# Kernel tuning notes

Hardware: AMD Instinct MI355X
Metric: run time of the kernel (lower is better)

Reference implementation:

```python
import jax, jax.numpy as jnp
import numpy as np

EPS = 1e-5


def _layernorm(x, w, b):
    mu = jnp.mean(x, axis=-1, keepdims=True)
    var = jnp.var(x, axis=-1, keepdims=True)
    return (x - mu) * jax.lax.rsqrt(var + EPS) * w + b


def setup_inputs() -> dict:
    key = jax.random.key(0)
    ks = jax.random.split(key, 3)
    h, dff = 1024, 4096
    x = jax.random.normal(ks[0], (4, 2048, h), dtype=jnp.float32)
    w1 = jax.random.normal(ks[1], (h, dff), dtype=jnp.float32) * (1.0 / np.sqrt(h))
    w2 = jax.random.normal(ks[2], (dff, h), dtype=jnp.float32) * (1.0 / np.sqrt(dff))
    return {
        "x": x,
        "ln1_w": jnp.ones((h,), jnp.float32),
        "ln1_b": jnp.zeros((h,), jnp.float32),
        "ln2_w": jnp.ones((h,), jnp.float32),
        "ln2_b": jnp.zeros((h,), jnp.float32),
        "w1": w1,
        "b1": jnp.zeros((dff,), jnp.float32),
        "w2": w2,
        "b2": jnp.zeros((h,), jnp.float32),
    }


def reference(x, ln1_w, ln1_b, ln2_w, ln2_b, w1, b1, w2, b2):
    # double 1D FFT: over hidden (dim=-1) then sequence (dim=-2), keep real part
    fourier_x = jnp.fft.fft(jnp.fft.fft(x, axis=-1), axis=-2).real
    x = x + fourier_x
    x = _layernorm(x, ln1_w, ln1_b)
    # FFN: Linear -> exact GELU -> Linear (dropout is identity in eval)
    h = jax.nn.gelu(jnp.einsum("bsd,df->bsf", x, w1) + b1, approximate=False)
    x = x + jnp.einsum("bsf,fd->bsd", h, w2) + b2
    return _layernorm(x, ln2_w, ln2_b)
```

## Files before the change

kernel.cpp:

```cpp
#include <hip/hip_runtime.h>
#include <hip/hip_bf16.h>
#include <math.h>

typedef __bf16 bf16_t;
typedef __bf16 bf16x8 __attribute__((ext_vector_type(8)));
typedef __bf16 bf16x4 __attribute__((ext_vector_type(4)));
typedef float  f32x4  __attribute__((ext_vector_type(4)));

#define NROWS 8192
#define HD    1024
#define DFF   4096
#define HKEEP 544

typedef __attribute__((address_space(1))) const void* gas_cptr;
typedef __attribute__((address_space(3))) void* las_ptr;

__device__ __forceinline__ void gload_lds16(const void* g, void* l) {
  __builtin_amdgcn_global_load_lds((gas_cptr)g, (las_ptr)l, 16, 0, 0);
}

__global__ __launch_bounds__(256) void transpose_to_bf16(
    const float* __restrict__ in, bf16_t* __restrict__ out, int R, int C)
{
  __shared__ float tile[32][33];
  const int bx = blockIdx.x, by = blockIdx.y;
  const int tx = threadIdx.x, ty = threadIdx.y;
  #pragma unroll
  for (int i = ty; i < 32; i += 8)
    tile[i][tx] = in[(size_t)(by*32 + i)*C + bx*32 + tx];
  __syncthreads();
  #pragma unroll
  for (int i = ty; i < 32; i += 8)
    out[(size_t)(bx*32 + i)*R + by*32 + tx] = (bf16_t)tile[tx][i];
}

__global__ __launch_bounds__(256) void fft_h_kernel(
    const float* __restrict__ x, float* __restrict__ re, float* __restrict__ im)
{
  __shared__ float sre[1024], sim[1024], twc[512], tws[512];
  const int t = threadIdx.x;
  const size_t row = blockIdx.x;
  const float* xr = x + row * HD;
  for (int k = t; k < 512; k += 256) {
    float sv, cv; sincosf(-6.28318530717958647692f * (float)k * (1.0f/1024.0f), &sv, &cv);
    twc[k] = cv; tws[k] = sv;
  }
  #pragma unroll
  for (int q = 0; q < 4; ++q) sre[t + 256*q] = xr[t + 256*q];
  __syncthreads();
  float rv[4];
  #pragma unroll
  for (int q = 0; q < 4; ++q) rv[q] = sre[__brev((unsigned)(t + 256*q)) >> 22];
  __syncthreads();
  #pragma unroll
  for (int q = 0; q < 4; ++q) { sre[t + 256*q] = rv[q]; sim[t + 256*q] = 0.0f; }
  __syncthreads();
  for (int s = 0; s < 10; ++s) {
    const int half = 1 << s;
    #pragma unroll
    for (int q = 0; q < 2; ++q) {
      const int b  = t + 256*q;
      const int j  = b & (half - 1);
      const int ib = ((b >> s) << (s + 1)) | j;
      const int ti2 = j << (9 - s);
      const float wc = twc[ti2], ws = tws[ti2];
      const float r1 = sre[ib],       i1v = sim[ib];
      const float r2 = sre[ib+half],  i2v = sim[ib+half];
      const float tr = r2*wc - i2v*ws;
      const float ti = r2*ws + i2v*wc;
      sre[ib]      = r1 + tr; sim[ib]      = i1v + ti;
      sre[ib+half] = r1 - tr; sim[ib+half] = i1v - ti;
    }
    __syncthreads();
  }
  #pragma unroll
  for (int q = 0; q < 4; ++q) {
    const int idx = t + 256*q;
    if (idx < HKEEP) {
      re[row*HD + idx] = sre[idx];
      im[row*HD + idx] = sim[idx];
    }
  }
}

__global__ __launch_bounds__(256) void transpose2_f32(
    const float* __restrict__ re, const float* __restrict__ im,
    float* __restrict__ reT, float* __restrict__ imT)
{
  __shared__ float t0[32][33], t1[32][33];
  const int h0 = blockIdx.x * 32;
  const int b0 = blockIdx.y * 32;
  const int tx = threadIdx.x, ty = threadIdx.y;
  #pragma unroll
  for (int i = ty; i < 32; i += 8) {
    t0[i][tx] = re[(size_t)(b0+i)*HD + h0+tx];
    t1[i][tx] = im[(size_t)(b0+i)*HD + h0+tx];
  }
  __syncthreads();
  #pragma unroll
  for (int i = ty; i < 32; i += 8) {
    reT[(size_t)(h0+i)*NROWS + b0+tx] = t0[tx][i];
    imT[(size_t)(h0+i)*NROWS + b0+tx] = t1[tx][i];
  }
}

__global__ __launch_bounds__(256) void fft_s_col(
    const float* __restrict__ reT, const float* __restrict__ imT,
    float* __restrict__ fT)
{
  __shared__ float sre[2048], sim[2048], twc[1024], tws[1024];
  const int t = threadIdx.x;
  const int h = blockIdx.x;
  const int batch = blockIdx.y;
  const size_t base = (size_t)h * NROWS + batch * 2048;
  for (int k = t; k < 1024; k += 256) {
    float sv, cv; sincosf(-6.28318530717958647692f * (float)k * (1.0f/2048.0f), &sv, &cv);
    twc[k] = cv; tws[k] = sv;
  }
  #pragma unroll
  for (int q = 0; q < 8; ++q) {
    const int i = t + 256*q;
    const int src = __brev((unsigned)i) >> 21;
    sre[i] = reT[base + src];
    sim[i] = imT[base + src];
  }
  __syncthreads();
  for (int s = 0; s < 11; ++s) {
    const int half = 1 << s;
    #pragma unroll
    for (int q = 0; q < 4; ++q) {
      const int b  = t + 256*q;
      const int j  = b & (half - 1);
      const int ib = ((b >> s) << (s + 1)) | j;
      const int ti2 = j << (10 - s);
      const float wc = twc[ti2], ws = tws[ti2];
      const float r1 = sre[ib],       i1v = sim[ib];
      const float r2 = sre[ib+half],  i2v = sim[ib+half];
      const float tr = r2*wc - i2v*ws;
      const float ti = r2*ws + i2v*wc;
      sre[ib]      = r1 + tr; sim[ib]      = i1v + ti;
      sre[ib+half] = r1 - tr; sim[ib+half] = i1v - ti;
    }
    __syncthreads();
  }
  #pragma unroll
  for (int q = 0; q < 8; ++q) {
    const int i = t + 256*q;
    fT[base + i] = sre[i];
  }
}

__global__ __launch_bounds__(256) void umadd_kernel(
    const float* __restrict__ fT, const float* __restrict__ x,
    float* __restrict__ y)
{
  __shared__ float tile[32][33];
  const int h0 = blockIdx.x * 32;
  const int b0 = blockIdx.y * 32;
  const int tx = threadIdx.x, ty = threadIdx.y;
  const int batch = b0 >> 11;
  const int s0    = b0 & 2047;
  #pragma unroll
  for (int i = ty; i < 32; i += 8) {
    const int h = h0 + i;
    float v;
    if (h <= 512) {
      v = fT[(size_t)h * NROWS + b0 + tx];
    } else {
      const int sp = (2048 - (s0 + tx)) & 2047;
      v = fT[(size_t)(1024 - h) * NROWS + (batch << 11) + sp];
    }
    tile[i][tx] = v;
  }
  __syncthreads();
  #pragma unroll
  for (int i = ty; i < 32; i += 8) {
    const size_t gi = (size_t)(b0+i)*HD + h0+tx;
    y[gi] = x[gi] + tile[tx][i];
  }
}

template <bool OUT_BF16>
__global__ __launch_bounds__(256) void layernorm_k(
    const float* __restrict__ in, const float* __restrict__ gw,
    const float* __restrict__ gb, bf16_t* __restrict__ ob, float* __restrict__ of)
{
  __shared__ float red[8];
  const size_t row = blockIdx.x;
  const int t = threadIdx.x;
  const float* xr = in + row * HD;
  float4 v = *(const float4*)(xr + t*4);
  float s = v.x + v.y + v.z + v.w;
  #pragma unroll
  for (int o = 32; o > 0; o >>= 1) s += __shfl_xor(s, o);
  if ((t & 63) == 0) red[t >> 6] = s;
  __syncthreads();
  const float mu = (red[0]+red[1]+red[2]+red[3]) * (1.0f/1024.0f);
  const float dx = v.x-mu, dy = v.y-mu, dz = v.z-mu, dw = v.w-mu;
  float sq = dx*dx + dy*dy + dz*dz + dw*dw;
  #pragma unroll
  for (int o = 32; o > 0; o >>= 1) sq += __shfl_xor(sq, o);
  if ((t & 63) == 0) red[4 + (t >> 6)] = sq;
  __syncthreads();
  const float var  = (red[4]+red[5]+red[6]+red[7]) * (1.0f/1024.0f);
  const float rstd = rsqrtf(var + 1e-5f);
  const float4 wv = *(const float4*)(gw + t*4);
  const float4 bv = *(const float4*)(gb + t*4);
  const float o0 = dx*rstd*wv.x + bv.x;
  const float o1 = dy*rstd*wv.y + bv.y;
  const float o2 = dz*rstd*wv.z + bv.z;
  const float o3 = dw*rstd*wv.w + bv.w;
  if constexpr (OUT_BF16) {
    bf16x4 o; o[0]=(bf16_t)o0; o[1]=(bf16_t)o1; o[2]=(bf16_t)o2; o[3]=(bf16_t)o3;
    *(bf16x4*)(ob + row*HD + t*4) = o;
  } else {
    float4 o; o.x=o0; o.y=o1; o.z=o2; o.w=o3;
    *(float4*)(of + row*HD + t*4) = o;
  }
}

__device__ __forceinline__ float gelu_exact(float v) {
  return 0.5f * v * (1.0f + erff(v * 0.70710678118654752440f));
}

template <bool GELU_BF16_OUT>
__global__ __launch_bounds__(256) void gemm_bf16_kernel(
    const bf16_t* __restrict__ A,
    const bf16_t* __restrict__ Bt,
    const float*  __restrict__ bias,
    const bf16_t* __restrict__ resid,
    bf16_t* __restrict__ outB, float* __restrict__ outF,
    int M, int N, int K, int gx)
{
  constexpr int BK = 64;
  __shared__ bf16_t As[128*BK];
  __shared__ bf16_t Bs[128*BK];
  const int tid  = threadIdx.x;
  const int wave = tid >> 6, lane = tid & 63;
  const int wr = wave >> 1, wc = wave & 1;
  const int lr  = lane & 15;
  const int lkg = lane >> 4;

  const int nwg = gridDim.x;
  const int sid = (blockIdx.x & 7) * (nwg >> 3) + (blockIdx.x >> 3);
  const int bx = sid % gx, by = sid / gx;
  const int brow = by * 128, bcol = bx * 128;

  const int rloc = lane >> 3;
  const int sgrp = (lane & 7) ^ rloc;
  const bf16_t* Ag = A  + (size_t)(brow + wave*32 + rloc) * K + sgrp * 8;
  const bf16_t* Bg = Bt + (size_t)(bcol + wave*32 + rloc) * K + sgrp * 8;

  f32x4 acc[4][4] = {};

  for (int k0 = 0; k0 < K; k0 += BK) {
    #pragma unroll
    for (int q = 0; q < 4; ++q) {
      gload_lds16(Ag + (size_t)(q*8)*K + k0, &As[(wave*4 + q) * 512]);
      gload_lds16(Bg + (size_t)(q*8)*K + k0, &Bs[(wave*4 + q) * 512]);
    }
    __syncthreads();

    #pragma unroll
    for (int ks = 0; ks < 2; ++ks) {
      const int g = (lkg + ks*4) ^ (lr & 7);
      bf16x8 af[4], bv[4];
      #pragma unroll
      for (int m = 0; m < 4; ++m)
        af[m] = *(const bf16x8*)&As[(wr*64 + m*16 + lr)*BK + g*8];
      #pragma unroll
      for (int n = 0; n < 4; ++n)
        bv[n] = *(const bf16x8*)&Bs[(wc*64 + n*16 + lr)*BK + g*8];
      #pragma unroll
      for (int m = 0; m < 4; ++m)
        #pragma unroll
        for (int n = 0; n < 4; ++n)
          acc[m][n] = __builtin_amdgcn_mfma_f32_16x16x32_bf16(bv[n], af[m], acc[m][n], 0, 0, 0);
    }
    __syncthreads();
  }

  #pragma unroll
  for (int m = 0; m < 4; ++m) {
    const int row = brow + wr*64 + m*16 + lr;
    #pragma unroll
    for (int n = 0; n < 4; ++n) {
      const int col = bcol + wc*64 + n*16 + lkg*4;
      const float4 bv4 = *(const float4*)(bias + col);
      float v0 = acc[m][n][0] + bv4.x;
      float v1 = acc[m][n][1] + bv4.y;
      float v2 = acc[m][n][2] + bv4.z;
      float v3 = acc[m][n][3] + bv4.w;
      if constexpr (GELU_BF16_OUT) {
        bf16x4 o;
        o[0] = (bf16_t)gelu_exact(v0); o[1] = (bf16_t)gelu_exact(v1);
        o[2] = (bf16_t)gelu_exact(v2); o[3] = (bf16_t)gelu_exact(v3);
        *(bf16x4*)(outB + (size_t)row * N + col) = o;
      } else {
        bf16x4 rr = *(const bf16x4*)(resid + (size_t)row * N + col);
        float4 o;
        o.x = v0 + (float)rr[0]; o.y = v1 + (float)rr[1];
        o.z = v2 + (float)rr[2]; o.w = v3 + (float)rr[3];
        *(float4*)(outF + (size_t)row * N + col) = o;
      }
    }
  }
}

extern "C" void kernel_launch(void* const* d_in, const int* in_sizes, int n_in,
                              void* d_out, int out_size, void* d_ws, size_t ws_size,
                              hipStream_t stream) {
  const float* x    = (const float*)d_in[0];
  const float* ln1w = (const float*)d_in[1];
  const float* ln1b = (const float*)d_in[2];
  const float* ln2w = (const float*)d_in[3];
  const float* ln2b = (const float*)d_in[4];
  const float* w1   = (const float*)d_in[5];
  const float* b1   = (const float*)d_in[6];
  const float* w2   = (const float*)d_in[7];
  const float* b2   = (const float*)d_in[8];
  float* out = (float*)d_out;

  char* ws = (char*)d_ws;
  bf16_t* w1b = (bf16_t*)(ws);
  bf16_t* w2b = (bf16_t*)(ws + (8u  << 20));
  float*  re  = (float*) (ws + (16u << 20));
  float*  im  = (float*) (ws + (48u << 20));
  float*  reT = (float*) (ws + (80u << 20));
  float*  imT = (float*) (ws + (98u << 20));
  float*  fT  = (float*) (ws + (16u << 20));
  float*  y   = (float*) (ws + (33u << 20));
  bf16_t* xn  = (bf16_t*)(ws + (16u << 20));
  bf16_t* hg  = (bf16_t*)(ws + (64u << 20));

  transpose_to_bf16<<<dim3(DFF/32, HD/32), dim3(32, 8), 0, stream>>>(w1, w1b, HD, DFF);
  transpose_to_bf16<<<dim3(HD/32, DFF/32), dim3(32, 8), 0, stream>>>(w2, w2b, DFF, HD);

  fft_h_kernel<<<NROWS, 256, 0, stream>>>(x, re, im);

  transpose2_f32<<<dim3(HKEEP/32, NROWS/32), dim3(32, 8), 0, stream>>>(re, im, reT, imT);

  fft_s_col<<<dim3(513, 4), 256, 0, stream>>>(reT, imT, fT);

  umadd_kernel<<<dim3(HD/32, NROWS/32), dim3(32, 8), 0, stream>>>(fT, x, y);

  layernorm_k<true><<<NROWS, 256, 0, stream>>>(y, ln1w, ln1b, xn, nullptr);

  gemm_bf16_kernel<true><<<(DFF/128)*(NROWS/128), 256, 0, stream>>>(
      xn, w1b, b1, nullptr, hg, nullptr, NROWS, DFF, HD, DFF/128);
  gemm_bf16_kernel<false><<<(HD/128)*(NROWS/128), 256, 0, stream>>>(
      hg, w2b, b2, xn, nullptr, out, NROWS, HD, DFF, HD/128);

  layernorm_k<false><<<NROWS, 256, 0, stream>>>(out, ln2w, ln2b, nullptr, out);
}
```

Before: 332.1 us.

## Rewrite FFN GEMMs as 8-wave double-buffered pipelined kernel with larger tiles

```diff
diff --git a/kernel.cpp b/kernel.cpp
--- a/kernel.cpp
+++ b/kernel.cpp
@@ -223,8 +223,8 @@
   return 0.5f * v * (1.0f + erff(v * 0.70710678118654752440f));
 }
 
-template <bool GELU_BF16_OUT>
-__global__ __launch_bounds__(256) void gemm_bf16_kernel(
+template <int NFRAG, bool GELU_OUT>
+__global__ __launch_bounds__(512, 2) void gemm8_kernel(
     const bf16_t* __restrict__ A,
     const bf16_t* __restrict__ Bt,
     const float*  __restrict__ bias,
@@ -232,66 +232,106 @@
     bf16_t* __restrict__ outB, float* __restrict__ outF,
     int M, int N, int K, int gx)
 {
-  constexpr int BK = 64;
-  __shared__ bf16_t As[128*BK];
-  __shared__ bf16_t Bs[128*BK];
+  constexpr int BN = NFRAG * 64;
+  constexpr int BH = BN / 2;
+  __shared__ bf16_t As[2][256 * 64];
+  __shared__ bf16_t Bs[2][BN * 64];
+
   const int tid  = threadIdx.x;
   const int wave = tid >> 6, lane = tid & 63;
-  const int wr = wave >> 1, wc = wave & 1;
-  const int lr  = lane & 15;
-  const int lkg = lane >> 4;
+  const int wr = wave >> 2, wc = wave & 3;
+  const int lr = lane & 15, lkg = lane >> 4;
 
   const int nwg = gridDim.x;
   const int sid = (blockIdx.x & 7) * (nwg >> 3) + (blockIdx.x >> 3);
   const int bx = sid % gx, by = sid / gx;
-  const int brow = by * 128, bcol = bx * 128;
-
-  const int rloc = lane >> 3;
-  const int sgrp = (lane & 7) ^ rloc;
-  const bf16_t* Ag = A  + (size_t)(brow + wave*32 + rloc) * K + sgrp * 8;
-  const bf16_t* Bg = Bt + (size_t)(bcol + wave*32 + rloc) * K + sgrp * 8;
-
-  f32x4 acc[4][4] = {};
-
-  for (int k0 = 0; k0 < K; k0 += BK) {
+  const int brow = by * 256, bcol = bx * BN;
+
+  const int rl = lane >> 3;
+  const int sg = (lane & 7) ^ rl;
+  const bf16_t* Abase = A  + (size_t)(brow + wave*8 + rl) * K + sg*8;
+  const bf16_t* Bbase = Bt + (size_t)(bcol + wave*8 + rl) * K + sg*8;
+
+  auto stageA = [&](int b, int h, int t) {
+    const bf16_t* g = Abase + (size_t)(h*128) * K + t*64;
+    bf16_t* l = &As[b][(h*128 + wave*8) * 64];
+    gload_lds16(g, l);
+    gload_lds16(g + (size_t)64 * K, l + 64*64);
+  };
+  auto stageB = [&](int b, int h, int t) {
+    const bf16_t* g = Bbase + (size_t)(h*BH) * K + t*64;
+    bf16_t* l = &Bs[b][(h*BH + wave*8) * 64];
+    gload_lds16(g, l);
+    if constexpr (NFRAG == 4)
+      gload_lds16(g + (size_t)64 * K, l + 64*64);
+  };
+
+  f32x4 acc[8][NFRAG] = {};
+  bf16x8 af[4], bv[NFRAG];
+
+  const int NT = K >> 6;
+  const int NI = NT >> 1;
+
+  stageA(0,0,0); stageA(0,1,0); stageB(0,0,0); stageB(0,1,0);
+  stageA(1,0,1); stageA(1,1,1); stageB(1,0,1); stageB(1,1,1);
+  asm volatile("s_waitcnt vmcnt(0)" ::: "memory");
+  __builtin_amdgcn_s_barrier();
+
+  #define RD_B(BUF, KS) _Pragma("unroll") \
+      for (int n = 0; n < NFRAG; ++n) { \
+        const int r = wc*(NFRAG*16) + n*16 + lr; \
+        bv[n] = *(const bf16x8*)&Bs[BUF][r*64 + (((lkg + KS*4) ^ (lr & 7))*8)]; }
+  #define RD_A(BUF, MH, KS) _Pragma("unroll") \
+      for (int m = 0; m < 4; ++m) { \
+        const int r = wr*128 + (MH*4 + m)*16 + lr; \
+        af[m] = *(const bf16x8*)&As[BUF][r*64 + (((lkg + KS*4) ^ (lr & 7))*8)]; }
+  #define MFMA_Q(MH) __builtin_amdgcn_s_setprio(1); \
+      _Pragma("unroll") \
+      for (int m = 0; m < 4; ++m) { \
+        _Pragma("unroll") \
+        for (int n = 0; n < NFRAG; ++n) \
+          acc[MH*4 + m][n] = __builtin_amdgcn_mfma_f32_16x16x32_bf16(bv[n], af[m], acc[MH*4 + m][n], 0, 0, 0); } \
+      __builtin_amdgcn_s_setprio(0);
+  #define BAR() __builtin_amdgcn_s_barrier()
+  #define LGKM0() asm volatile("s_waitcnt lgkmcnt(0)" ::: "memory")
+  #define VMW() do { if constexpr (NFRAG == 4) asm volatile("s_waitcnt vmcnt(2)" ::: "memory"); \
+                     else                      asm volatile("s_waitcnt vmcnt(1)" ::: "memory"); } while(0)
+
+  for (int j = 0; j < NI; ++j) {
+    const int t1 = 2*j + 1;
+    const int t2 = (2*j + 2 < NT) ? 2*j + 2 : NT - 1;
+    const int t3 = (2*j + 3 < NT) ? 2*j + 3 : NT - 1;
+
+    RD_B(0,0); RD_A(0,0,0); stageB(1,1,t1);
+    BAR(); LGKM0(); MFMA_Q(0); BAR();
+    RD_A(0,1,0); stageA(1,0,t1);
+    BAR(); LGKM0(); MFMA_Q(1); BAR();
+    RD_B(0,1); RD_A(0,0,1); stageA(1,1,t1);
+    BAR(); LGKM0(); MFMA_Q(0); BAR();
+    RD_A(0,1,1); stageB(0,0,t2);
+    BAR(); LGKM0(); MFMA_Q(1); VMW(); BAR();
+    RD_B(1,0); RD_A(1,0,0); stageB(0,1,t2);
+    BAR(); LGKM0(); MFMA_Q(0); BAR();
+    RD_A(1,1,0); stageA(0,0,t2);
+    BAR(); LGKM0(); MFMA_Q(1); BAR();
+    RD_B(1,1); RD_A(1,0,1); stageA(0,1,t2);
+    BAR(); LGKM0(); MFMA_Q(0); BAR();
+    RD_A(1,1,1); stageB(1,0,t3);
+    BAR(); LGKM0(); MFMA_Q(1); VMW(); BAR();
+  }
+
+  #pragma unroll
+  for (int m = 0; m < 8; ++m) {
+    const int row = brow + wr*128 + m*16 + lr;
     #pragma unroll
-    for (int q = 0; q < 4; ++q) {
-      gload_lds16(Ag + (size_t)(q*8)*K + k0, &As[(wave*4 + q) * 512]);
-      gload_lds16(Bg + (size_t)(q*8)*K + k0, &Bs[(wave*4 + q) * 512]);
-    }
-    __syncthreads();
-
-    #pragma unroll
-    for (int ks = 0; ks < 2; ++ks) {
-      const int g = (lkg + ks*4) ^ (lr & 7);
-      bf16x8 af[4], bv[4];
-      #pragma unroll
-      for (int m = 0; m < 4; ++m)
-        af[m] = *(const bf16x8*)&As[(wr*64 + m*16 + lr)*BK + g*8];
-      #pragma unroll
-      for (int n = 0; n < 4; ++n)
-        bv[n] = *(const bf16x8*)&Bs[(wc*64 + n*16 + lr)*BK + g*8];
-      #pragma unroll
-      for (int m = 0; m < 4; ++m)
-        #pragma unroll
-        for (int n = 0; n < 4; ++n)
-          acc[m][n] = __builtin_amdgcn_mfma_f32_16x16x32_bf16(bv[n], af[m], acc[m][n], 0, 0, 0);
-    }
-    __syncthreads();
-  }
-
-  #pragma unroll
-  for (int m = 0; m < 4; ++m) {
-    const int row = brow + wr*64 + m*16 + lr;
-    #pragma unroll
-    for (int n = 0; n < 4; ++n) {
-      const int col = bcol + wc*64 + n*16 + lkg*4;
+    for (int n = 0; n < NFRAG; ++n) {
+      const int col = bcol + wc*(NFRAG*16) + n*16 + lkg*4;
       const float4 bv4 = *(const float4*)(bias + col);
       float v0 = acc[m][n][0] + bv4.x;
       float v1 = acc[m][n][1] + bv4.y;
       float v2 = acc[m][n][2] + bv4.z;
       float v3 = acc[m][n][3] + bv4.w;
-      if constexpr (GELU_BF16_OUT) {
+      if constexpr (GELU_OUT) {
         bf16x4 o;
         o[0] = (bf16_t)gelu_exact(v0); o[1] = (bf16_t)gelu_exact(v1);
         o[2] = (bf16_t)gelu_exact(v2); o[3] = (bf16_t)gelu_exact(v3);
@@ -305,6 +345,12 @@
       }
     }
   }
+  #undef RD_B
+  #undef RD_A
+  #undef MFMA_Q
+  #undef BAR
+  #undef LGKM0
+  #undef VMW
 }
 
 extern "C" void kernel_launch(void* const* d_in, const int* in_sizes, int n_in,
@@ -346,9 +392,9 @@
 
   layernorm_k<true><<<NROWS, 256, 0, stream>>>(y, ln1w, ln1b, xn, nullptr);
 
-  gemm_bf16_kernel<true><<<(DFF/128)*(NROWS/128), 256, 0, stream>>>(
-      xn, w1b, b1, nullptr, hg, nullptr, NROWS, DFF, HD, DFF/128);
-  gemm_bf16_kernel<false><<<(HD/128)*(NROWS/128), 256, 0, stream>>>(
+  gemm8_kernel<4, true><<<(DFF/256)*(NROWS/256), 512, 0, stream>>>(
+      xn, w1b, b1, nullptr, hg, nullptr, NROWS, DFF, HD, DFF/256);
+  gemm8_kernel<2, false><<<(HD/128)*(NROWS/256), 512, 0, stream>>>(
       hg, w2b, b2, xn, nullptr, out, NROWS, HD, DFF, HD/128);
 
   layernorm_k<false><<<NROWS, 256, 0, stream>>>(out, ln2w, ln2b, nullptr, out);
```

Result: slower. 376.2 us (+13.3%).

## Fuse hidden-dim FFT with transpose and use tanh-approx GELU

Applied to the files above, without the earlier changes.

```diff
diff --git a/kernel.cpp b/kernel.cpp
--- a/kernel.cpp
+++ b/kernel.cpp
@@ -10,7 +10,7 @@
 #define NROWS 8192
 #define HD    1024
 #define DFF   4096
-#define HKEEP 544
+#define HKEEP 513
 
 typedef __attribute__((address_space(1))) const void* gas_cptr;
 typedef __attribute__((address_space(3))) void* las_ptr;
@@ -34,73 +34,69 @@
     out[(size_t)(bx*32 + i)*R + by*32 + tx] = (bf16_t)tile[tx][i];
 }
 
-__global__ __launch_bounds__(256) void fft_h_kernel(
-    const float* __restrict__ x, float* __restrict__ re, float* __restrict__ im)
-{
-  __shared__ float sre[1024], sim[1024], twc[512], tws[512];
+#define RPB 16
+#define LDW 1036
+__global__ __launch_bounds__(512) void fft_h_t(
+    const float* __restrict__ x, float* __restrict__ reT, float* __restrict__ imT)
+{
+  __shared__ float sre[RPB*LDW], sim[RPB*LDW], twc[512], tws[512];
   const int t = threadIdx.x;
-  const size_t row = blockIdx.x;
-  const float* xr = x + row * HD;
-  for (int k = t; k < 512; k += 256) {
-    float sv, cv; sincosf(-6.28318530717958647692f * (float)k * (1.0f/1024.0f), &sv, &cv);
-    twc[k] = cv; tws[k] = sv;
-  }
-  #pragma unroll
-  for (int q = 0; q < 4; ++q) sre[t + 256*q] = xr[t + 256*q];
-  __syncthreads();
-  float rv[4];
-  #pragma unroll
-  for (int q = 0; q < 4; ++q) rv[q] = sre[__brev((unsigned)(t + 256*q)) >> 22];
-  __syncthreads();
-  #pragma unroll
-  for (int q = 0; q < 4; ++q) { sre[t + 256*q] = rv[q]; sim[t + 256*q] = 0.0f; }
+  const int row0 = blockIdx.x * RPB;
+  {
+    float sv, cv; sincosf(-6.28318530717958647692f * (float)t * (1.0f/1024.0f), &sv, &cv);
+    twc[t] = cv; tws[t] = sv;
+  }
+  #pragma unroll
+  for (int q = 0; q < 8; ++q) {
+    const int i = t + 512*q;
+    const int row = i >> 8, c4 = i & 255;
+    float4 v = *(const float4*)(x + (size_t)(row0+row)*HD + c4*4);
+    *(float4*)&sre[row*LDW + c4*4] = v;
+  }
+  __syncthreads();
+  const int b0i = __brev((unsigned)t) >> 22;
+  const int b1i = __brev((unsigned)(t + 512)) >> 22;
+  float rv[32];
+  #pragma unroll
+  for (int q = 0; q < 16; ++q) {
+    rv[2*q]   = sre[q*LDW + b0i];
+    rv[2*q+1] = sre[q*LDW + b1i];
+  }
+  __syncthreads();
+  #pragma unroll
+  for (int q = 0; q < 16; ++q) {
+    sre[q*LDW + t]       = rv[2*q];
+    sre[q*LDW + t + 512] = rv[2*q+1];
+    sim[q*LDW + t]       = 0.0f;
+    sim[q*LDW + t + 512] = 0.0f;
+  }
   __syncthreads();
   for (int s = 0; s < 10; ++s) {
     const int half = 1 << s;
-    #pragma unroll
-    for (int q = 0; q < 2; ++q) {
-      const int b  = t + 256*q;
-      const int j  = b & (half - 1);
-      const int ib = ((b >> s) << (s + 1)) | j;
-      const int ti2 = j << (9 - s);
-      const float wc = twc[ti2], ws = tws[ti2];
-      const float r1 = sre[ib],       i1v = sim[ib];
-      const float r2 = sre[ib+half],  i2v = sim[ib+half];
+    const int j    = t & (half - 1);
+    const int ib   = ((t >> s) << (s + 1)) | j;
+    const int ti2  = j << (9 - s);
+    const float wc = twc[ti2], ws = tws[ti2];
+    #pragma unroll
+    for (int q = 0; q < 16; ++q) {
+      float* pr = &sre[q*LDW]; float* pi = &sim[q*LDW];
+      const float r1 = pr[ib],      i1v = pi[ib];
+      const float r2 = pr[ib+half], i2v = pi[ib+half];
       const float tr = r2*wc - i2v*ws;
       const float ti = r2*ws + i2v*wc;
-      sre[ib]      = r1 + tr; sim[ib]      = i1v + ti;
-      sre[ib+half] = r1 - tr; sim[ib+half] = i1v - ti;
+      pr[ib]      = r1 + tr; pi[ib]      = i1v + ti;
+      pr[ib+half] = r1 - tr; pi[ib+half] = i1v - ti;
     }
     __syncthreads();
   }
-  #pragma unroll
-  for (int q = 0; q < 4; ++q) {
-    const int idx = t + 256*q;
-    if (idx < HKEEP) {
-      re[row*HD + idx] = sre[idx];
-      im[row*HD + idx] = sim[idx];
-    }
-  }
-}
-
-__global__ __launch_bounds__(256) void transpose2_f32(
-    const float* __restrict__ re, const float* __restrict__ im,
-    float* __restrict__ reT, float* __restrict__ imT)
-{
-  __shared__ float t0[32][33], t1[32][33];
-  const int h0 = blockIdx.x * 32;
-  const int b0 = blockIdx.y * 32;
-  const int tx = threadIdx.x, ty = threadIdx.y;
-  #pragma unroll
-  for (int i = ty; i < 32; i += 8) {
-    t0[i][tx] = re[(size_t)(b0+i)*HD + h0+tx];
-    t1[i][tx] = im[(size_t)(b0+i)*HD + h0+tx];
-  }
-  __syncthreads();
-  #pragma unroll
-  for (int i = ty; i < 32; i += 8) {
-    reT[(size_t)(h0+i)*NROWS + b0+tx] = t0[tx][i];
-    imT[(size_t)(h0+i)*NROWS + b0+tx] = t1[tx][i];
+  const int tx = t & 15, th = t >> 4;
+  #pragma unroll
+  for (int hh = 0; hh < 17; ++hh) {
+    const int h = hh*32 + th;
+    if (h < HKEEP) {
+      reT[(size_t)h*NROWS + row0 + tx] = sre[tx*LDW + h];
+      imT[(size_t)h*NROWS + row0 + tx] = sim[tx*LDW + h];
+    }
   }
 }
 
@@ -219,8 +215,10 @@
   }
 }
 
-__device__ __forceinline__ float gelu_exact(float v) {
-  return 0.5f * v * (1.0f + erff(v * 0.70710678118654752440f));
+__device__ __forceinline__ float gelu_fast(float v) {
+  const float u  = 0.7978845608028654f * v * (1.0f + 0.044715f * v * v);
+  const float e  = exp2f(-2.8853900817779268f * u);
+  return v / (1.0f + e);
 }
 
 template <bool GELU_BF16_OUT>
@@ -293,8 +291,8 @@
       float v3 = acc[m][n][3] + bv4.w;
       if constexpr (GELU_BF16_OUT) {
         bf16x4 o;
-        o[0] = (bf16_t)gelu_exact(v0); o[1] = (bf16_t)gelu_exact(v1);
-        o[2] = (bf16_t)gelu_exact(v2); o[3] = (bf16_t)gelu_exact(v3);
+        o[0] = (bf16_t)gelu_fast(v0); o[1] = (bf16_t)gelu_fast(v1);
+        o[2] = (bf16_t)gelu_fast(v2); o[3] = (bf16_t)gelu_fast(v3);
         *(bf16x4*)(outB + (size_t)row * N + col) = o;
       } else {
         bf16x4 rr = *(const bf16x4*)(resid + (size_t)row * N + col);
@@ -324,21 +322,17 @@
   char* ws = (char*)d_ws;
   bf16_t* w1b = (bf16_t*)(ws);
   bf16_t* w2b = (bf16_t*)(ws + (8u  << 20));
-  float*  re  = (float*) (ws + (16u << 20));
-  float*  im  = (float*) (ws + (48u << 20));
-  float*  reT = (float*) (ws + (80u << 20));
-  float*  imT = (float*) (ws + (98u << 20));
-  float*  fT  = (float*) (ws + (16u << 20));
-  float*  y   = (float*) (ws + (33u << 20));
-  bf16_t* xn  = (bf16_t*)(ws + (16u << 20));
-  bf16_t* hg  = (bf16_t*)(ws + (64u << 20));
+  float*  reT = (float*) (ws + (16u << 20));
+  float*  imT = (float*) (ws + (33u << 20));
+  float*  fT  = (float*) (ws + (50u << 20));
+  float*  y   = (float*) (ws + (67u << 20));
+  bf16_t* xn  = (bf16_t*)(ws + (99u << 20));
+  bf16_t* hg  = (bf16_t*)(ws + (16u << 20));
 
   transpose_to_bf16<<<dim3(DFF/32, HD/32), dim3(32, 8), 0, stream>>>(w1, w1b, HD, DFF);
   transpose_to_bf16<<<dim3(HD/32, DFF/32), dim3(32, 8), 0, stream>>>(w2, w2b, DFF, HD);
 
-  fft_h_kernel<<<NROWS, 256, 0, stream>>>(x, re, im);
-
-  transpose2_f32<<<dim3(HKEEP/32, NROWS/32), dim3(32, 8), 0, stream>>>(re, im, reT, imT);
+  fft_h_t<<<NROWS/RPB, 512, 0, stream>>>(x, reT, imT);
 
   fft_s_col<<<dim3(513, 4), 256, 0, stream>>>(reT, imT, fT);
 
```

New measurement: 326.9 us. Within noise of the previous version (-1.6%).
